# Performance work log

Measured on AMD Instinct MI355X. Metric: run time of the kernel, lower is better.

## Reference

```python
import jax, jax.numpy as jnp
import numpy as np

B, T, N, C = 32, 12, 1024, 64
NW = T - 3   # number of 4-step windows (9)
K = 4        # window length == res_filters[0]
NL = 3       # len(filters)


def setup_inputs() -> dict:
    key = jax.random.key(0)
    ks = jax.random.split(key, 9)
    s = 0.02
    return {
        "original_data": jax.random.normal(ks[0], (B, T, N, C), jnp.float32),
        "data": jax.random.normal(ks[1], (B, T, N, C), jnp.float32),
        "adj_st": jax.random.uniform(ks[2], (N, 4 * N), jnp.float32) / (4.0 * N),
        "temporal_emb": jax.random.normal(ks[3], (1, T, 1, C), jnp.float32) * s,
        "spatial_emb": jax.random.normal(ks[4], (1, 1, N, C), jnp.float32) * s,
        "conv1_w": jax.random.normal(ks[5], (2 * C, C, 1, K), jnp.float32) * s,
        "conv1_b": jax.random.normal(ks[6], (2 * C,), jnp.float32) * s,
        "gcn_w": jax.random.normal(ks[7], (NW, NL, C, 2 * C), jnp.float32) * s,
        "gcn_b": jax.random.normal(ks[8], (NW, NL, 1, 2 * C), jnp.float32) * 0.1,
    }


def reference(original_data, data, adj_st, temporal_emb, spatial_emb,
              conv1_w, conv1_b, gcn_w, gcn_b):
    # ---- residual gated conv along time axis (T==12 so conv2 branch is dead) ----
    temp = jnp.transpose(data, (0, 3, 2, 1))  # (B,C,N,T)
    temp = jax.lax.conv_general_dilated(
        temp, conv1_w, window_strides=(1, 1), padding="VALID",
        dimension_numbers=("NCHW", "OIHW", "NCHW"))  # (B,2C,N,T-K+1)
    temp = temp + conv1_b[None, :, None, None]
    left, right = temp[:, :C], temp[:, C:]
    data_res = jnp.transpose(jax.nn.sigmoid(left) * right, (0, 3, 2, 1))  # (B,NW,N,C)

    # ---- position embedding (add) ----
    x = data + temporal_emb + spatial_emb  # (B,T,N,C)

    # ---- build all 4-step windows: (NW, 4N, B, C) ----
    idx = jnp.arange(NW)[:, None] + jnp.arange(K)[None, :]  # (NW,K)
    wins = x[:, idx]                                         # (B,NW,K,N,C)
    wins = jnp.transpose(wins, (1, 2, 3, 0, 4)).reshape(NW, K * N, B, C)

    def one_window(win, Ws, bs):
        wing, cur = win[:3 * N], win[3 * N:]
        outs = []
        for j in range(NL):
            full = jnp.concatenate([wing, cur], axis=0)       # (4N,B,C)
            y = jnp.einsum("nm,mbc->nbc", adj_st, full)       # (N,B,C)
            z = jnp.einsum("nbc,cd->nbd", y, Ws[j]) + bs[j]   # (N,B,2C)
            cur = z[..., :C] * jax.nn.sigmoid(z[..., C:])      # GLU
            outs.append(cur)
        return jnp.max(jnp.stack(outs, 0), axis=0)            # (N,B,C)

    out = jax.vmap(one_window)(wins, gcn_w, gcn_b)            # (NW,N,B,C)
    out = jnp.transpose(out, (2, 0, 1, 3))                    # (B,NW,N,C)
    return out + data_res
```

## Files before the change

### kernel.cpp

```cpp
#include <hip/hip_runtime.h>
#include <cstdint>
#include <cstddef>


typedef __bf16 bf16;
typedef float f32x4 __attribute__((ext_vector_type(4)));
typedef __bf16 bf16x8 __attribute__((ext_vector_type(8)));
typedef __bf16 bf16x4 __attribute__((ext_vector_type(4)));

constexpr int B_  = 32;
constexpr int T_  = 12;
constexpr int N_  = 1024;
constexpr int C_  = 64;
constexpr int NW_ = 9;
constexpr long long SLAB_ = 2048LL * 1024LL;

constexpr int OF_ADJ  = 0;
constexpr int OF_TEMB = 4194304;
constexpr int OF_SEMB = 4195072;
constexpr int OF_C1W  = 4260608;
constexpr int OF_C1B  = 4293376;
constexpr int OF_GW   = 4293504;
constexpr int OF_GB   = 4514688;
constexpr int OF_END  = 4518144;

static __device__ __forceinline__ float sigmoidf_(float x) {
  return __builtin_amdgcn_rcpf(1.0f + __expf(-x));
}

static __device__ __forceinline__ void g2l16(const bf16* g, bf16* l) {
  __builtin_amdgcn_global_load_lds(
      (const __attribute__((address_space(1))) void*)g,
      (__attribute__((address_space(3))) void*)l, 16, 0, 0);
}

__global__ __launch_bounds__(256)
void k_detect(const void* __restrict__ data_raw, int* __restrict__ flag)
{
  __shared__ int cnt;
  const int tid = threadIdx.x;
  if (tid == 0) cnt = 0;
  __syncthreads();
  const uint32_t* W = (const uint32_t*)data_raw;
  int local = 0;
  for (int s = 0; s < 32; s++) {
    const uint32_t w = W[tid * 32 + s];
    const int e8 = (int)((w >> 7) & 0xFF);
    local += (e8 < 97 || e8 > 157) ? 1 : 0;
  }
  atomicAdd(&cnt, local);
  __syncthreads();
  if (tid == 0) *flag = (cnt > 2458) ? 1 : 0;
}

static __device__ __forceinline__ float rd_(const void* p, long long i, int isF32) {
  return isF32 ? ((const float*)p)[i] : (float)((const bf16*)p)[i];
}

__global__ __launch_bounds__(256)
void k_convert(const void* adj, const void* temb, const void* semb,
               const void* c1w, const void* c1b, const void* gw, const void* gb,
               const int* __restrict__ flagp, bf16* __restrict__ canon)
{
  const int isF32 = *flagp;
  const int e = blockIdx.x * 256 + threadIdx.x;
  float v;
  if      (e < OF_TEMB) v = rd_(adj,  e,           isF32);
  else if (e < OF_SEMB) v = rd_(temb, e - OF_TEMB, isF32);
  else if (e < OF_C1W)  v = rd_(semb, e - OF_SEMB, isF32);
  else if (e < OF_C1B)  v = rd_(c1w,  e - OF_C1W,  isF32);
  else if (e < OF_GW)   v = rd_(c1b,  e - OF_C1B,  isF32);
  else if (e < OF_GB)   v = rd_(gw,   e - OF_GW,   isF32);
  else                  v = rd_(gb,   e - OF_GB,   isF32);
  canon[e] = (bf16)v;
}

__global__ __launch_bounds__(256)
void k_prepg(const void* __restrict__ data_raw, const int* __restrict__ flagp,
             const bf16* __restrict__ temb, const bf16* __restrict__ semb,
             bf16* __restrict__ xg, int tbase)
{
  const int isF32 = *flagp;
  const int s  = blockIdx.z;
  const int t  = tbase + s;
  const int n0 = blockIdx.x * 32;
  const int bc = blockIdx.y * 256 + threadIdx.x;
  const int b = bc >> 6, c = bc & 63;

  __shared__ bf16 lsS[32 * 64];
  *(bf16x8*)&lsS[threadIdx.x * 8] = *(const bf16x8*)&semb[n0 * C_ + threadIdx.x * 8];
  __syncthreads();

  const float te = (float)temb[t * C_ + c];
  const long long dbase = ((long long)(b * T_ + t) * N_ + n0) * C_ + c;
  bf16* op = xg + (size_t)s * SLAB_ + (size_t)bc * N_ + n0;
#pragma unroll
  for (int i = 0; i < 32; i += 8) {
    bf16x8 v;
#pragma unroll
    for (int u = 0; u < 8; u++) {
      const int n = i + u;
      const float dv = rd_(data_raw, dbase + (long long)n * C_, isF32);
      v[u] = (bf16)(dv + te + (float)lsS[n * C_ + c]);
    }
    *(bf16x8*)&op[i] = v;
  }
}

__global__ __launch_bounds__(256)
void k_wprep(const bf16* __restrict__ conv1w, const bf16* __restrict__ gcnw,
             bf16* __restrict__ Wt, bf16* __restrict__ gwT)
{
  const int idx = blockIdx.x * 256 + threadIdx.x;
  if (idx < 128 * 256) {
    const int c2 = idx >> 8, kidx = idx & 255;
    const int ci = kidx & 63, k = kidx >> 6;
    Wt[idx] = conv1w[c2 * 256 + ci * 4 + k];
  }
  const int i2 = idx - 128 * 256;
  if (i2 >= 0 && i2 < 27 * 8192) {
    const int wj = i2 >> 13, r = i2 & 8191;
    const int d = r >> 6, c = r & 63;
    gwT[i2] = gcnw[wj * 8192 + c * 128 + d];
  }
}

template<int MODE>
__global__ __launch_bounds__(256)
void k_gemm_adj(const bf16* __restrict__ Aadj, const bf16* __restrict__ Bop,
                const float* __restrict__ initY, float* __restrict__ outF,
                const bf16* __restrict__ gwT, const bf16* __restrict__ gcnb,
                bf16* __restrict__ outCur, int Ksize, int jlayer, int wbase)
{
  const int lw = blockIdx.z;
  const int m0 = blockIdx.y * 128;
  const int c0 = blockIdx.x * 128;
  const int tid = threadIdx.x;
  const int lane = tid & 63, wid = tid >> 6;
  const int lrow = lane & 15, q = lane >> 4;
  const int wm = wid >> 1, wn = wid & 1;

  __shared__ __align__(16) bf16 lsAll[16384];

  const int srow = lane >> 2;
  const int sl_w = ((lane >> 2) & 3) ^ ((lane >> 4) & 3);
  const int skel = ((lane & 3) ^ sl_w) * 8;

  const int sl_r  = (lrow & 3) ^ (lrow >> 2);
  const int rdoff = ((q ^ sl_r) & 3) * 8;

  const bf16* Bw = Bop + (size_t)lw * SLAB_;

  auto STAGE = [&](int buf, int k0) {
    const int tblk = k0 >> 10;
    const int kloc = k0 & 1023;
    const bf16* Bt = Bw + (size_t)tblk * SLAB_ + kloc;
    const bf16* At = Aadj + k0;
#pragma unroll
    for (int s = 0; s < 2; s++) {
      const int ch  = s * 4 + wid;
      const int row = ch * 16 + srow;
      g2l16(&At[(size_t)(m0 + row) * 4096 + skel], &lsAll[buf * 4096 + ch * 512]);
      g2l16(&Bt[(size_t)(c0 + row) * N_   + skel], &lsAll[8192 + buf * 4096 + ch * 512]);
    }
  };

  STAGE(0, 0);

  f32x4 acc[4][4];
  const size_t woff = (size_t)lw * SLAB_;
  if (MODE == 1) {
#pragma unroll
    for (int i = 0; i < 4; i++)
#pragma unroll
      for (int jj = 0; jj < 4; jj++) {
        const int col = c0 + wn * 64 + jj * 16 + lrow;
        const int b = col >> 6, c = col & 63;
        const float* yp = initY + woff + (size_t)b * (N_ * C_)
                        + (size_t)(m0 + wm * 64 + i * 16 + q * 4) * C_ + c;
#pragma unroll
        for (int r = 0; r < 4; r++) acc[i][jj][r] = yp[(size_t)r * C_];
      }
  } else {
#pragma unroll
    for (int i = 0; i < 4; i++)
#pragma unroll
      for (int jj = 0; jj < 4; jj++)
#pragma unroll
        for (int r = 0; r < 4; r++) acc[i][jj][r] = 0.0f;
  }

  __syncthreads();

  int cur = 0;
  for (int k0 = 0; k0 < Ksize; k0 += 32) {
    if (k0 + 32 < Ksize) STAGE(cur ^ 1, k0 + 32);

    bf16x8 af[4], bfv[4];
#pragma unroll
    for (int i = 0; i < 4; i++)
      af[i]  = *(const bf16x8*)&lsAll[cur * 4096 + (wm * 64 + i * 16 + lrow) * 32 + rdoff];
#pragma unroll
    for (int jj = 0; jj < 4; jj++)
      bfv[jj] = *(const bf16x8*)&lsAll[8192 + cur * 4096 + (wn * 64 + jj * 16 + lrow) * 32 + rdoff];
#pragma unroll
    for (int i = 0; i < 4; i++)
#pragma unroll
      for (int jj = 0; jj < 4; jj++)
        acc[i][jj] = __builtin_amdgcn_mfma_f32_16x16x32_bf16(af[i], bfv[jj], acc[i][jj], 0, 0, 0);

    __syncthreads();
    cur ^= 1;
  }

  if (MODE == 0) {
#pragma unroll
    for (int i = 0; i < 4; i++)
#pragma unroll
      for (int jj = 0; jj < 4; jj++) {
        const int col = c0 + wn * 64 + jj * 16 + lrow;
        const int b = col >> 6, c = col & 63;
        const size_t base = woff + (size_t)b * (N_ * C_)
                          + (size_t)(m0 + wm * 64 + i * 16 + q * 4) * C_ + c;
#pragma unroll
        for (int r = 0; r < 4; r++) outF[base + (size_t)r * C_] = acc[i][jj][r];
      }
    return;
  }

  char* tls = (char*)lsAll;
#pragma unroll
  for (int i = 0; i < 4; i++)
#pragma unroll
    for (int jj = 0; jj < 4; jj++) {
      const int bc = wn * 64 + jj * 16 + lrow;
#pragma unroll
      for (int r = 0; r < 4; r++) {
        const int m = wm * 64 + i * 16 + q * 4 + r;
        const int byte = m * 256 + ((bc * 2) ^ (((m ^ (m >> 3)) & 7) << 4));
        *(bf16*)(tls + byte) = (bf16)acc[i][jj][r];
      }
    }
  __syncthreads();

  const int wj = (wbase + lw) * 3 + jlayer;
  const bf16* Agw  = gwT  + (size_t)wj * 8192;
  const bf16* bias = gcnb + (size_t)wj * 128;
  const int nloc0 = wid * 32;

#pragma unroll
  for (int bl = 0; bl < 2; bl++) {
    f32x4 acc2[8][2];
#pragma unroll
    for (int rt = 0; rt < 8; rt++)
#pragma unroll
      for (int ct = 0; ct < 2; ct++)
#pragma unroll
        for (int r = 0; r < 4; r++) acc2[rt][ct][r] = 0.0f;

#pragma unroll
    for (int ks = 0; ks < 2; ks++) {
      bf16x8 bv[2];
#pragma unroll
      for (int ct = 0; ct < 2; ct++) {
        const int nl = nloc0 + ct * 16 + lrow;
        const int byte = nl * 256 +
          (((bl * 64 + ks * 32 + q * 8) * 2) ^ (((nl ^ (nl >> 3)) & 7) << 4));
        bv[ct] = *(const bf16x8*)(tls + byte);
      }
#pragma unroll
      for (int rt = 0; rt < 8; rt++) {
        const bf16x8 av = *(const bf16x8*)&Agw[(rt * 16 + lrow) * 64 + ks * 32 + q * 8];
#pragma unroll
        for (int ct = 0; ct < 2; ct++)
          acc2[rt][ct] = __builtin_amdgcn_mfma_f32_16x16x32_bf16(av, bv[ct], acc2[rt][ct], 0, 0, 0);
      }
    }

    const int bg = (c0 >> 6) + bl;
#pragma unroll
    for (int rt = 0; rt < 4; rt++)
#pragma unroll
      for (int ct = 0; ct < 2; ct++) {
        const int n = m0 + nloc0 + ct * 16 + lrow;
#pragma unroll
        for (int r = 0; r < 4; r++) {
          const int d = rt * 16 + q * 4 + r;
          const float zL = acc2[rt][ct][r]     + (float)bias[d];
          const float zR = acc2[rt + 4][ct][r] + (float)bias[d + 64];
          const float cv = zL * sigmoidf_(zR);
          outCur[woff + (size_t)(bg * 64 + d) * N_ + n] = (bf16)cv;
        }
      }
  }
}

__global__ __launch_bounds__(256)
void k_final(const void* __restrict__ data_raw, const int* __restrict__ flagp,
             const bf16* __restrict__ Wt, const bf16* __restrict__ convb,
             const bf16* __restrict__ cur0, const bf16* __restrict__ cur1,
             const bf16* __restrict__ cur2, float* __restrict__ out, int wbase)
{
  const int isF32 = *flagp;
  const int lw = blockIdx.z;
  const int w = wbase + lw;
  const int bbat = blockIdx.y;
  const int tid = threadIdx.x;
  const int lane = tid & 63, wid = tid >> 6;
  const int lrow = lane & 15, q = lane >> 4;
  const int n0 = blockIdx.x * 128 + wid * 32;

  f32x4 acc[2][8];
#pragma unroll
  for (int rt = 0; rt < 2; rt++)
#pragma unroll
    for (int ct = 0; ct < 8; ct++)
#pragma unroll
      for (int r = 0; r < 4; r++) acc[rt][ct][r] = 0.0f;

#pragma unroll
  for (int s = 0; s < 8; s++) {
    const int k = s >> 1, ci0 = (s & 1) * 32;
    bf16x8 av[2];
#pragma unroll
    for (int rt = 0; rt < 2; rt++) {
      const long long off =
        ((long long)((bbat * T_ + w + k) * N_) + n0 + rt * 16 + lrow) * C_ + ci0 + q * 8;
      if (!isF32) {
        av[rt] = *(const bf16x8*)&((const bf16*)data_raw)[off];
      } else {
        const float* p = (const float*)data_raw + off;
        const f32x4 v0 = *(const f32x4*)p;
        const f32x4 v1 = *(const f32x4*)(p + 4);
        bf16x8 v;
#pragma unroll
        for (int u = 0; u < 4; u++) { v[u] = (bf16)v0[u]; v[u + 4] = (bf16)v1[u]; }
        av[rt] = v;
      }
    }
#pragma unroll
    for (int ct = 0; ct < 8; ct++) {
      const bf16x8 bv = *(const bf16x8*)&Wt[(ct * 16 + lrow) * 256 + s * 32 + q * 8];
#pragma unroll
      for (int rt = 0; rt < 2; rt++)
        acc[rt][ct] = __builtin_amdgcn_mfma_f32_16x16x32_bf16(av[rt], bv, acc[rt][ct], 0, 0, 0);
    }
  }

#pragma unroll
  for (int rt = 0; rt < 2; rt++)
#pragma unroll
    for (int ctL = 0; ctL < 4; ctL++) {
      const int cL = ctL * 16 + lrow;
      const float bL = (float)convb[cL], bR = (float)convb[cL + 64];
      const size_t cbase = (size_t)lw * SLAB_ + (size_t)(bbat * 64 + cL) * N_
                         + n0 + rt * 16 + q * 4;
      const bf16x4 m0v = *(const bf16x4*)&cur0[cbase];
      const bf16x4 m1v = *(const bf16x4*)&cur1[cbase];
      const bf16x4 m2v = *(const bf16x4*)&cur2[cbase];
#pragma unroll
      for (int r = 0; r < 4; r++) {
        const int n = n0 + rt * 16 + q * 4 + r;
        const float zL = acc[rt][ctL][r] + bL;
        const float zR = acc[rt][ctL + 4][r] + bR;
        const float res = sigmoidf_(zL) * zR;
        const float mv = fmaxf(fmaxf((float)m0v[r], (float)m1v[r]), (float)m2v[r]);
        out[(size_t)((bbat * NW_ + w) * N_ + n) * C_ + cL] = res + mv;
      }
    }
}

extern "C" void kernel_launch(void* const* d_in, const int* in_sizes, int n_in,
                              void* d_out, int out_size, void* d_ws, size_t ws_size,
                              hipStream_t stream)
{
  (void)in_sizes; (void)n_in; (void)out_size;
  const void* data   = d_in[1];
  const void* adj    = d_in[2];
  const void* temb   = d_in[3];
  const void* semb   = d_in[4];
  const void* conv1w = d_in[5];
  const void* conv1b = d_in[6];
  const void* gcnw   = d_in[7];
  const void* gcnb   = d_in[8];
  float* out = (float*)d_out;

  auto fpn = [&](int g) -> size_t {
    size_t need = 256;
    auto pad = [&](size_t x) { need += (x + 255) & ~(size_t)255; };
    pad((size_t)OF_END * 2);
    pad((size_t)(g + 3) * SLAB_ * 2);
    pad((size_t)g * SLAB_ * 4);
    pad((size_t)3 * g * SLAB_ * 2);
    pad(128 * 256 * 2);
    pad(27 * 8192 * 2);
    return need;
  };

  int G = 1;
  for (int g = 9; g >= 2; g--) if (fpn(g) <= ws_size) { G = g; break; }

  char* ws = (char*)d_ws;
  int* flag = (int*)ws;
  size_t off = 256;
  auto allocB = [&](size_t bytes) -> char* {
    char* p = ws + off;
    off += (bytes + 255) & ~(size_t)255;
    return p;
  };
  bf16*  canon = (bf16*) allocB((size_t)OF_END * 2);
  bf16*  xg    = (bf16*) allocB((size_t)(G + 3) * SLAB_ * 2);
  float* Yw    = (float*)allocB((size_t)G * SLAB_ * 4);
  bf16*  curT  = (bf16*) allocB((size_t)3 * G * SLAB_ * 2);
  bf16*  Wt    = (bf16*) allocB(128 * 256 * 2);
  bf16*  gwT   = (bf16*) allocB(27 * 8192 * 2);

  bf16* cur0 = curT;
  bf16* cur1 = curT + (size_t)G * SLAB_;
  bf16* cur2 = curT + (size_t)2 * G * SLAB_;

  const bf16* adjC  = canon + OF_ADJ;
  const bf16* tembC = canon + OF_TEMB;
  const bf16* sembC = canon + OF_SEMB;
  const bf16* c1wC  = canon + OF_C1W;
  const bf16* c1bC  = canon + OF_C1B;
  const bf16* gwC   = canon + OF_GW;
  const bf16* gbC   = canon + OF_GB;

  k_detect<<<dim3(1), 256, 0, stream>>>(data, flag);
  k_convert<<<dim3(OF_END / 256), 256, 0, stream>>>(adj, temb, semb, conv1w, conv1b,
                                                    gcnw, gcnb, flag, canon);
  k_wprep<<<dim3(992), 256, 0, stream>>>(c1wC, gwC, Wt, gwT);

  for (int wbase = 0; wbase < NW_; wbase += G) {
    const int gc = (NW_ - wbase < G) ? (NW_ - wbase) : G;

    k_prepg<<<dim3(32, 8, gc + 3), 256, 0, stream>>>(data, flag, tembC, sembC, xg, wbase);

    k_gemm_adj<0><<<dim3(16, 8, gc), 256, 0, stream>>>(
        adjC, xg, nullptr, Yw, nullptr, nullptr, nullptr, 3072, 0, 0);

    k_gemm_adj<1><<<dim3(16, 8, gc), 256, 0, stream>>>(
        adjC + 3072, xg + 3 * SLAB_, Yw, nullptr, gwT, gbC, cur0, 1024, 0, wbase);
    k_gemm_adj<1><<<dim3(16, 8, gc), 256, 0, stream>>>(
        adjC + 3072, cur0, Yw, nullptr, gwT, gbC, cur1, 1024, 1, wbase);
    k_gemm_adj<1><<<dim3(16, 8, gc), 256, 0, stream>>>(
        adjC + 3072, cur1, Yw, nullptr, gwT, gbC, cur2, 1024, 2, wbase);

    k_final<<<dim3(8, 32, gc), 256, 0, stream>>>(data, flag, Wt, c1bC,
                                                 cur0, cur1, cur2, out, wbase);
  }
}
```

Baseline: 854.2 us.

## Stage data time slab in LDS in k_final and store Yw transposed

k_final now loads one batch's full 12-step slab for 32 nodes into swizzled LDS once and reuses it across all windows in the group. Each wave keeps its conv weight fragments in registers and handles one 16-channel L/R pair, so the grid is no longer split by window. Separately, the MODE 0/1 GEMM writes and reads the partial-sum buffer Yw in a (col, node) layout so each access is one f32x4 vector. The intent is to cut redundant global reads of overlapping windows and scattered scalar accesses, at the cost of fewer, longer-running blocks in k_final.

```diff
diff --git a/kernel.cpp b/kernel.cpp
--- a/kernel.cpp
+++ b/kernel.cpp
@@ -175,11 +175,8 @@
 #pragma unroll
       for (int jj = 0; jj < 4; jj++) {
         const int col = c0 + wn * 64 + jj * 16 + lrow;
-        const int b = col >> 6, c = col & 63;
-        const float* yp = initY + woff + (size_t)b * (N_ * C_)
-                        + (size_t)(m0 + wm * 64 + i * 16 + q * 4) * C_ + c;
-#pragma unroll
-        for (int r = 0; r < 4; r++) acc[i][jj][r] = yp[(size_t)r * C_];
+        const int m = m0 + wm * 64 + i * 16 + q * 4;
+        acc[i][jj] = *(const f32x4*)&initY[woff + (size_t)col * N_ + m];
       }
   } else {
 #pragma unroll
@@ -219,11 +216,8 @@
 #pragma unroll
       for (int jj = 0; jj < 4; jj++) {
         const int col = c0 + wn * 64 + jj * 16 + lrow;
-        const int b = col >> 6, c = col & 63;
-        const size_t base = woff + (size_t)b * (N_ * C_)
-                          + (size_t)(m0 + wm * 64 + i * 16 + q * 4) * C_ + c;
-#pragma unroll
-        for (int r = 0; r < 4; r++) outF[base + (size_t)r * C_] = acc[i][jj][r];
+        const int m = m0 + wm * 64 + i * 16 + q * 4;
+        *(f32x4*)&outF[woff + (size_t)col * N_ + m] = acc[i][jj];
       }
     return;
   }
@@ -299,61 +293,87 @@
 void k_final(const void* __restrict__ data_raw, const int* __restrict__ flagp,
              const bf16* __restrict__ Wt, const bf16* __restrict__ convb,
              const bf16* __restrict__ cur0, const bf16* __restrict__ cur1,
-             const bf16* __restrict__ cur2, float* __restrict__ out, int wbase)
+             const bf16* __restrict__ cur2, float* __restrict__ out,
+             int wbase, int gc)
 {
   const int isF32 = *flagp;
-  const int lw = blockIdx.z;
-  const int w = wbase + lw;
-  const int bbat = blockIdx.y;
+  const int b  = blockIdx.y;
+  const int n0 = blockIdx.x * 32;
   const int tid = threadIdx.x;
   const int lane = tid & 63, wid = tid >> 6;
   const int lrow = lane & 15, q = lane >> 4;
-  const int n0 = blockIdx.x * 128 + wid * 32;
-
-  f32x4 acc[2][8];
-#pragma unroll
-  for (int rt = 0; rt < 2; rt++)
-#pragma unroll
-    for (int ct = 0; ct < 8; ct++)
-#pragma unroll
-      for (int r = 0; r < 4; r++) acc[rt][ct][r] = 0.0f;
-
+
+  __shared__ __align__(16) bf16 lsD[T_ * 32 * C_];
+
+#pragma unroll
+  for (int it = 0; it < 6; it++) {
+    const int idx  = it * 256 + tid;
+    const int row  = idx >> 2;
+    const int part = idx & 3;
+    const int t = row >> 5, n = row & 31;
+    const long long goff = ((long long)(b * T_ + t) * N_ + n0 + n) * C_ + part * 16;
+    bf16x8 h0, h1;
+    if (isF32) {
+      const float* p = (const float*)data_raw + goff;
+      const f32x4 v0 = *(const f32x4*)p,      v1 = *(const f32x4*)(p + 4);
+      const f32x4 v2 = *(const f32x4*)(p + 8), v3 = *(const f32x4*)(p + 12);
+#pragma unroll
+      for (int u = 0; u < 4; u++) {
+        h0[u] = (bf16)v0[u]; h0[u + 4] = (bf16)v1[u];
+        h1[u] = (bf16)v2[u]; h1[u + 4] = (bf16)v3[u];
+      }
+    } else {
+      const bf16* p = (const bf16*)data_raw + goff;
+      h0 = *(const bf16x8*)p;
+      h1 = *(const bf16x8*)(p + 8);
+    }
+    const int base = row * 128 + part * 32;
+    const int swz  = (n & 7) << 4;
+    *(bf16x8*)((char*)lsD + (base ^ swz))        = h0;
+    *(bf16x8*)((char*)lsD + ((base + 16) ^ swz)) = h1;
+  }
+
+  bf16x8 bvL[8], bvR[8];
 #pragma unroll
   for (int s = 0; s < 8; s++) {
-    const int k = s >> 1, ci0 = (s & 1) * 32;
-    bf16x8 av[2];
+    bvL[s] = *(const bf16x8*)&Wt[(wid * 16 + lrow) * 256 + s * 32 + q * 8];
+    bvR[s] = *(const bf16x8*)&Wt[((wid + 4) * 16 + lrow) * 256 + s * 32 + q * 8];
+  }
+  const int cL = wid * 16 + lrow;
+  const float bL = (float)convb[cL], bR = (float)convb[cL + 64];
+
+  __syncthreads();
+
+  for (int wl = 0; wl < gc; wl++) {
+    const int w = wbase + wl;
+    f32x4 acc[2][2];
+#pragma unroll
+    for (int rt = 0; rt < 2; rt++)
+#pragma unroll
+      for (int ct = 0; ct < 2; ct++)
+#pragma unroll
+        for (int r = 0; r < 4; r++) acc[rt][ct][r] = 0.0f;
+
+#pragma unroll
+    for (int s = 0; s < 8; s++) {
+      const int t = w + (s >> 1), ci0 = (s & 1) * 32;
+      bf16x8 av[2];
+#pragma unroll
+      for (int rt = 0; rt < 2; rt++) {
+        const int n = rt * 16 + lrow;
+        const int byte = ((t * 32 + n) * 128 + (ci0 + q * 8) * 2) ^ ((n & 7) << 4);
+        av[rt] = *(const bf16x8*)((const char*)lsD + byte);
+      }
+#pragma unroll
+      for (int rt = 0; rt < 2; rt++) {
+        acc[rt][0] = __builtin_amdgcn_mfma_f32_16x16x32_bf16(av[rt], bvL[s], acc[rt][0], 0, 0, 0);
+        acc[rt][1] = __builtin_amdgcn_mfma_f32_16x16x32_bf16(av[rt], bvR[s], acc[rt][1], 0, 0, 0);
+      }
+    }
+
 #pragma unroll
     for (int rt = 0; rt < 2; rt++) {
-      const long long off =
-        ((long long)((bbat * T_ + w + k) * N_) + n0 + rt * 16 + lrow) * C_ + ci0 + q * 8;
-      if (!isF32) {
-        av[rt] = *(const bf16x8*)&((const bf16*)data_raw)[off];
-      } else {
-        const float* p = (const float*)data_raw + off;
-        const f32x4 v0 = *(const f32x4*)p;
-        const f32x4 v1 = *(const f32x4*)(p + 4);
-        bf16x8 v;
-#pragma unroll
-        for (int u = 0; u < 4; u++) { v[u] = (bf16)v0[u]; v[u + 4] = (bf16)v1[u]; }
-        av[rt] = v;
-      }
-    }
-#pragma unroll
-    for (int ct = 0; ct < 8; ct++) {
-      const bf16x8 bv = *(const bf16x8*)&Wt[(ct * 16 + lrow) * 256 + s * 32 + q * 8];
-#pragma unroll
-      for (int rt = 0; rt < 2; rt++)
-        acc[rt][ct] = __builtin_amdgcn_mfma_f32_16x16x32_bf16(av[rt], bv, acc[rt][ct], 0, 0, 0);
-    }
-  }
-
-#pragma unroll
-  for (int rt = 0; rt < 2; rt++)
-#pragma unroll
-    for (int ctL = 0; ctL < 4; ctL++) {
-      const int cL = ctL * 16 + lrow;
-      const float bL = (float)convb[cL], bR = (float)convb[cL + 64];
-      const size_t cbase = (size_t)lw * SLAB_ + (size_t)(bbat * 64 + cL) * N_
+      const size_t cbase = (size_t)wl * SLAB_ + (size_t)(b * 64 + cL) * N_
                          + n0 + rt * 16 + q * 4;
       const bf16x4 m0v = *(const bf16x4*)&cur0[cbase];
       const bf16x4 m1v = *(const bf16x4*)&cur1[cbase];
@@ -361,13 +381,14 @@
 #pragma unroll
       for (int r = 0; r < 4; r++) {
         const int n = n0 + rt * 16 + q * 4 + r;
-        const float zL = acc[rt][ctL][r] + bL;
-        const float zR = acc[rt][ctL + 4][r] + bR;
+        const float zL = acc[rt][0][r] + bL;
+        const float zR = acc[rt][1][r] + bR;
         const float res = sigmoidf_(zL) * zR;
         const float mv = fmaxf(fmaxf((float)m0v[r], (float)m1v[r]), (float)m2v[r]);
-        out[(size_t)((bbat * NW_ + w) * N_ + n) * C_ + cL] = res + mv;
-      }
-    }
+        out[(size_t)((b * NW_ + w) * N_ + n) * C_ + cL] = res + mv;
+      }
+    }
+  }
 }
 
 extern "C" void kernel_launch(void* const* d_in, const int* in_sizes, int n_in,
@@ -447,7 +468,7 @@
     k_gemm_adj<1><<<dim3(16, 8, gc), 256, 0, stream>>>(
         adjC + 3072, cur1, Yw, nullptr, gwT, gbC, cur2, 1024, 2, wbase);
 
-    k_final<<<dim3(8, 32, gc), 256, 0, stream>>>(data, flag, Wt, c1bC,
-                                                 cur0, cur1, cur2, out, wbase);
-  }
-}
+    k_final<<<dim3(32, 32, 1), 256, 0, stream>>>(data, flag, Wt, c1bC,
+                                                 cur0, cur1, cur2, out, wbase, gc);
+  }
+}
```

Result: faster. 749.7 us (-12.2%).
